# Optimization experiments

Hardware: AMD Instinct MI355X
Metric: run time of the kernel (lower is better)

## Reference

```python
import jax, jax.numpy as jnp
import numpy as np
from jax import lax

DIM = 384
NH = 8
HD = DIM // NH
M = 16          # num_anchors
B = 16
HH = 64
WW = 64
N = HH * WW
STD = 0.02


def setup_inputs() -> dict:
    key = jax.random.key(0)
    ks = jax.random.split(key, 12)
    rn = lambda k, shape: (jax.random.normal(k, shape, jnp.float32) * STD)
    return {
        "x": jax.random.normal(ks[0], (B, N, DIM), jnp.float32),
        "H": HH,
        "W": WW,
        "saliency_w": rn(ks[1], (DIM, 1)),
        "saliency_b": jnp.zeros((1,), jnp.float32),
        "anchor_seeds": rn(ks[2], (1, M, DIM)),
        "w_q_agg": rn(ks[3], (DIM, DIM)),
        "w_kv_agg": rn(ks[4], (DIM, 2 * DIM)),
        "w_q_self": rn(ks[5], (DIM, DIM)),
        "w_kv_self": rn(ks[6], (DIM, 2 * DIM)),
        "w_q_bcast": rn(ks[7], (DIM, DIM)),
        "w_kv_bcast": rn(ks[8], (DIM, 2 * DIM)),
        "dw_kernel": rn(ks[9], (DIM, 1, 3, 3)),  # depthwise conv, OIHW with I=1
        "w_proj": rn(ks[10], (DIM, DIM)),
    }


def _mhsa(q_in, kv_in, wq, wkv):
    """Multi-head cross attention. q_in: [B,Lq,C], kv_in: [B,Lk,C]."""
    b, lq, c = q_in.shape
    lk = kv_in.shape[1]
    scale = HD ** -0.5
    q = (q_in @ wq).reshape(b, lq, NH, HD)
    kv = (kv_in @ wkv).reshape(b, lk, 2, NH, HD)
    k, v = kv[:, :, 0], kv[:, :, 1]
    attn = jnp.einsum("bqhd,bkhd->bhqk", q, k) * scale
    attn = jax.nn.softmax(attn, axis=-1)
    out = jnp.einsum("bhqk,bkhd->bqhd", attn, v).reshape(b, lq, c)
    return out


def reference(x, H, W, saliency_w, saliency_b, anchor_seeds,
              w_q_agg, w_kv_agg, w_q_self, w_kv_self,
              w_q_bcast, w_kv_bcast, dw_kernel, w_proj):
    b, n, c = x.shape
    # saliency gating
    sal = jax.nn.sigmoid(x @ saliency_w + saliency_b)  # [B,N,1]
    x_sal = x * sal
    # stage 1: anchors aggregate from saliency-gated tokens
    anchors = jnp.broadcast_to(anchor_seeds, (b, M, c))
    anchors = anchors + _mhsa(anchors, x_sal, w_q_agg, w_kv_agg)
    # stage 2: anchor self-attention
    anchors = anchors + _mhsa(anchors, anchors, w_q_self, w_kv_self)
    # stage 3: broadcast anchors back to all tokens
    global_out = _mhsa(x, anchors, w_q_bcast, w_kv_bcast)
    # depthwise 3x3 conv on the 2D token map
    x2d = x.reshape(b, H, W, c).transpose(0, 3, 1, 2)  # NCHW
    local = lax.conv_general_dilated(
        x2d, dw_kernel, window_strides=(1, 1), padding="SAME",
        feature_group_count=c,
        dimension_numbers=("NCHW", "OIHW", "NCHW"))
    local = local.transpose(0, 2, 3, 1).reshape(b, n, c)
    return (global_out + local) @ w_proj
```

## Files before the change

kernel.cpp:

```cpp
#include <hip/hip_runtime.h>
#include <hip/hip_bf16.h>

#define SCALE 0.14433756729740643f

typedef __attribute__((ext_vector_type(8))) short bf16x8;
typedef __attribute__((ext_vector_type(4))) float f32x4;

template <typename T> __device__ inline T cvt_from_f(float v);
template <> __device__ inline float cvt_from_f<float>(float v) { return v; }
template <> __device__ inline __hip_bfloat16 cvt_from_f<__hip_bfloat16>(float v) { return __float2bfloat16(v); }

__device__ inline void gload16(const void* g, void* l) {
  __builtin_amdgcn_global_load_lds((const __attribute__((address_space(1))) void*)g,
                                   (__attribute__((address_space(3))) void*)l, 16, 0, 0);
}

__device__ inline int xcd_flat(int nwg) {
  int flat = (blockIdx.z * gridDim.y + blockIdx.y) * gridDim.x + blockIdx.x;
  int per = nwg >> 3;
  return (flat & 7) * per + (flat >> 3);
}

__global__ __launch_bounds__(256) void prep(const float* __restrict__ x,
                                            const float* __restrict__ wsal,
                                            const float* __restrict__ bsal,
                                            __hip_bfloat16* __restrict__ xb,
                                            float* __restrict__ sal) {
  int wave = threadIdx.x >> 6, lane = threadIdx.x & 63;
  size_t row = (size_t)blockIdx.x * 4 + wave;
  const float* xr = x + row * 384;
  float xs[6];
  float part = 0.f;
#pragma unroll
  for (int j = 0; j < 6; j++) {
    int c = lane + 64 * j;
    xs[j] = xr[c];
    part += xs[j] * wsal[c];
  }
#pragma unroll
  for (int off = 32; off >= 1; off >>= 1) part += __shfl_xor(part, off);
  float s = 1.f / (1.f + __expf(-(part + bsal[0])));
#pragma unroll
  for (int j = 0; j < 6; j++) {
    int c = lane + 64 * j;
    xb[row * 384 + c] = __float2bfloat16(xs[j]);
  }
  if (lane == 0) sal[row] = s;
}

__global__ void wcast_tv(const float* __restrict__ w, __hip_bfloat16* __restrict__ wt) {
  int idx = blockIdx.x * 256 + threadIdx.x;
  if (idx >= 384 * 384) return;
  int n = idx / 384, k = idx % 384;
  wt[idx] = __float2bfloat16(w[(size_t)k * 768 + 384 + n]);
}

template <int K, typename OT, int BSHIFT>
__global__ __launch_bounds__(256) void gemm_mfma(const __hip_bfloat16* __restrict__ A,
                                                 const __hip_bfloat16* __restrict__ BT,
                                                 OT* __restrict__ out, int Ncols,
                                                 size_t btBatchStride) {
  __shared__ __align__(16) __hip_bfloat16 Asl[128][32];
  __shared__ __align__(16) __hip_bfloat16 Bsl[128][32];
  int nf = xcd_flat(gridDim.x * gridDim.y);
  int bX = nf % gridDim.x, bY = nf / gridDim.x;
  int tid = threadIdx.x;
  int lane = tid & 63;
  int w = tid >> 6;
  int wr = w >> 1, wc = w & 1;
  int fr = lane & 15, fq = lane >> 4;
  int rowBase = bY * 128, colBase = bX * 128;
  const __hip_bfloat16* BTb = BT + (size_t)(rowBase >> BSHIFT) * btBatchStride;

  int r1 = tid >> 2, kc1 = tid & 3;
  int r2 = (tid + 256) >> 2;

  char* aB1 = (char*)Asl + (size_t)(w * 64) * 16;
  char* aB2 = (char*)Asl + (size_t)(256 + w * 64) * 16;
  char* bB1 = (char*)Bsl + (size_t)(w * 64) * 16;
  char* bB2 = (char*)Bsl + (size_t)(256 + w * 64) * 16;

  const __hip_bfloat16* a1 = A + (size_t)(rowBase + r1) * K + kc1 * 8;
  const __hip_bfloat16* a2 = A + (size_t)(rowBase + r2) * K + kc1 * 8;
  const __hip_bfloat16* b1 = BTb + (size_t)(colBase + r1) * K + kc1 * 8;
  const __hip_bfloat16* b2 = BTb + (size_t)(colBase + r2) * K + kc1 * 8;

  f32x4 acc[4][4] = {};

  for (int kk = 0; kk < K; kk += 32) {
    gload16(a1 + kk, aB1);
    gload16(a2 + kk, aB2);
    gload16(b1 + kk, bB1);
    gload16(b2 + kk, bB2);
    __syncthreads();
    bf16x8 af[4], bfv[4];
#pragma unroll
    for (int m = 0; m < 4; m++) af[m] = *(const bf16x8*)&Asl[wr * 64 + m * 16 + fr][fq * 8];
#pragma unroll
    for (int n = 0; n < 4; n++) bfv[n] = *(const bf16x8*)&Bsl[wc * 64 + n * 16 + fr][fq * 8];
#pragma unroll
    for (int m = 0; m < 4; m++)
#pragma unroll
      for (int n = 0; n < 4; n++)
        acc[m][n] = __builtin_amdgcn_mfma_f32_16x16x32_bf16(af[m], bfv[n], acc[m][n], 0, 0, 0);
    __syncthreads();
  }

#pragma unroll
  for (int m = 0; m < 4; m++) {
    int row0 = rowBase + wr * 64 + m * 16 + fq * 4;
#pragma unroll
    for (int n = 0; n < 4; n++) {
      int col = colBase + wc * 64 + n * 16 + fr;
      f32x4 v = acc[m][n];
#pragma unroll
      for (int r = 0; r < 4; r++) out[(size_t)(row0 + r) * Ncols + col] = cvt_from_f<OT>(v[r]);
    }
  }
}

__global__ __launch_bounds__(256) void gemm_logits(const __hip_bfloat16* __restrict__ A,
                                                   const __hip_bfloat16* __restrict__ BT,
                                                   __hip_bfloat16* __restrict__ lgT,
                                                   const float* __restrict__ rowScale) {
  constexpr int K = 384;
  __shared__ __align__(16) __hip_bfloat16 Asl[128][32];
  __shared__ __align__(16) __hip_bfloat16 Bsl[128][32];
  int tid = threadIdx.x;
  int lane = tid & 63;
  int w = tid >> 6;
  int wr = w >> 1, wc = w & 1;
  int fr = lane & 15, fq = lane >> 4;
  int rowBase = blockIdx.x * 128;

  int r1 = tid >> 2, kc1 = tid & 3;
  int r2 = (tid + 256) >> 2;

  char* aB1 = (char*)Asl + (size_t)(w * 64) * 16;
  char* aB2 = (char*)Asl + (size_t)(256 + w * 64) * 16;
  char* bB1 = (char*)Bsl + (size_t)(w * 64) * 16;
  char* bB2 = (char*)Bsl + (size_t)(256 + w * 64) * 16;

  const __hip_bfloat16* a1 = A + (size_t)(rowBase + r1) * K + kc1 * 8;
  const __hip_bfloat16* a2 = A + (size_t)(rowBase + r2) * K + kc1 * 8;
  const __hip_bfloat16* b1 = BT + (size_t)r1 * K + kc1 * 8;
  const __hip_bfloat16* b2 = BT + (size_t)r2 * K + kc1 * 8;

  f32x4 acc[4][4] = {};

  for (int kk = 0; kk < K; kk += 32) {
    gload16(a1 + kk, aB1);
    gload16(a2 + kk, aB2);
    gload16(b1 + kk, bB1);
    gload16(b2 + kk, bB2);
    __syncthreads();
    bf16x8 af[4], bfv[4];
#pragma unroll
    for (int m = 0; m < 4; m++) af[m] = *(const bf16x8*)&Asl[wr * 64 + m * 16 + fr][fq * 8];
#pragma unroll
    for (int n = 0; n < 4; n++) bfv[n] = *(const bf16x8*)&Bsl[wc * 64 + n * 16 + fr][fq * 8];
#pragma unroll
    for (int m = 0; m < 4; m++)
#pragma unroll
      for (int n = 0; n < 4; n++)
        acc[m][n] = __builtin_amdgcn_mfma_f32_16x16x32_bf16(af[m], bfv[n], acc[m][n], 0, 0, 0);
    __syncthreads();
  }

  float sv[4][4];
#pragma unroll
  for (int m = 0; m < 4; m++)
#pragma unroll
    for (int r = 0; r < 4; r++)
      sv[m][r] = rowScale[rowBase + wr * 64 + m * 16 + fq * 4 + r];

#pragma unroll
  for (int m = 0; m < 4; m++) {
    int row0 = rowBase + wr * 64 + m * 16 + fq * 4;
    int bb = row0 >> 12;
    int n0 = row0 & 4095;
#pragma unroll
    for (int n = 0; n < 4; n++) {
      int col = wc * 64 + n * 16 + fr;
      __hip_bfloat16 tb[4];
#pragma unroll
      for (int r = 0; r < 4; r++) tb[r] = __float2bfloat16(acc[m][n][r] * sv[m][r]);
      *(unsigned long long*)(lgT + ((size_t)bb * 128 + col) * 4096 + n0) = *(unsigned long long*)tb;
    }
  }
}

__global__ __launch_bounds__(256) void softmax_rows(const __hip_bfloat16* __restrict__ lgT,
                                                    const float* __restrict__ sal,
                                                    __hip_bfloat16* __restrict__ PT) {
  int g = blockIdx.x;
  const __hip_bfloat16* row = lgT + (size_t)g * 4096;
  int tid = threadIdx.x, wv = tid >> 6, lane = tid & 63;
  __shared__ float redm[4], reds[4];
  float v[16];
  union { ulonglong2 u; __hip_bfloat16 h[8]; } L0, L1;
  L0.u = *(const ulonglong2*)(row + tid * 16);
  L1.u = *(const ulonglong2*)(row + tid * 16 + 8);
#pragma unroll
  for (int i = 0; i < 8; i++) {
    v[i] = __bfloat162float(L0.h[i]);
    v[8 + i] = __bfloat162float(L1.h[i]);
  }
  float mx = v[0];
#pragma unroll
  for (int i = 1; i < 16; i++) mx = fmaxf(mx, v[i]);
#pragma unroll
  for (int off = 1; off < 64; off <<= 1) mx = fmaxf(mx, __shfl_xor(mx, off));
  if (lane == 0) redm[wv] = mx;
  __syncthreads();
  mx = fmaxf(fmaxf(redm[0], redm[1]), fmaxf(redm[2], redm[3]));
  float s = 0.f;
#pragma unroll
  for (int i = 0; i < 16; i++) {
    v[i] = __expf(v[i] - mx);
    s += v[i];
  }
#pragma unroll
  for (int off = 1; off < 64; off <<= 1) s += __shfl_xor(s, off);
  if (lane == 0) reds[wv] = s;
  __syncthreads();
  s = (reds[0] + reds[1]) + (reds[2] + reds[3]);
  float inv = 1.f / s;
  const float* sp = sal + (size_t)(g >> 7) * 4096 + tid * 16;
  float salv[16];
#pragma unroll
  for (int i = 0; i < 4; i++) {
    float4 q = *(const float4*)(sp + i * 4);
    salv[i * 4] = q.x; salv[i * 4 + 1] = q.y; salv[i * 4 + 2] = q.z; salv[i * 4 + 3] = q.w;
  }
  __hip_bfloat16 tb[16];
#pragma unroll
  for (int i = 0; i < 16; i++) tb[i] = __float2bfloat16(v[i] * inv * salv[i]);
  __hip_bfloat16* op = PT + (size_t)g * 4096 + tid * 16;
  *(ulonglong2*)op = *(ulonglong2*)tb;
  *(ulonglong2*)(op + 8) = *(ulonglong2*)(tb + 8);
}

__global__ __launch_bounds__(256) void gemm_pvx(const __hip_bfloat16* __restrict__ PT,
                                                const __hip_bfloat16* __restrict__ xb,
                                                float* __restrict__ pbuf) {
  __shared__ __align__(16) __hip_bfloat16 Asl[128][32];
  __shared__ __align__(16) short Bsl[128][40];
  int nf = xcd_flat(384);
  int bX = nf % 3, bY = (nf / 3) & 15, kz = nf / 48;
  int tid = threadIdx.x;
  int lane = tid & 63;
  int w = tid >> 6;
  int wr = w >> 1, wc = w & 1;
  int fr = lane & 15, fq = lane >> 4;
  int rowBase = bY * 128, colBase = bX * 128;

  int r1 = tid >> 2, kc1 = tid & 3;
  int r2 = (tid + 256) >> 2;
  char* aB1 = (char*)Asl + (size_t)(w * 64) * 16;
  char* aB2 = (char*)Asl + (size_t)(256 + w * 64) * 16;
  const __hip_bfloat16* a1 = PT + (size_t)(rowBase + r1) * 4096 + kz * 512 + kc1 * 8;
  const __hip_bfloat16* a2 = PT + (size_t)(rowBase + r2) * 4096 + kz * 512 + kc1 * 8;

  int nl1 = tid >> 4;
  int cc = tid & 15;
  const __hip_bfloat16* Bg0 = xb + ((size_t)bY * 4096 + kz * 512) * 384 + colBase + cc * 8;

  f32x4 acc[4][4] = {};

  for (int kk = 0; kk < 512; kk += 32) {
    gload16(a1 + kk, aB1);
    gload16(a2 + kk, aB2);
    const __hip_bfloat16* Bg = Bg0 + (size_t)kk * 384;
    bf16x8 rb1 = *(const bf16x8*)(Bg + (size_t)nl1 * 384);
    bf16x8 rb2 = *(const bf16x8*)(Bg + (size_t)(nl1 + 16) * 384);
#pragma unroll
    for (int j = 0; j < 8; j++) {
      Bsl[cc * 8 + j][nl1] = rb1[j];
      Bsl[cc * 8 + j][nl1 + 16] = rb2[j];
    }
    __syncthreads();
    bf16x8 af[4], bfv[4];
#pragma unroll
    for (int m = 0; m < 4; m++) af[m] = *(const bf16x8*)&Asl[wr * 64 + m * 16 + fr][fq * 8];
#pragma unroll
    for (int n = 0; n < 4; n++) bfv[n] = *(const bf16x8*)&Bsl[wc * 64 + n * 16 + fr][fq * 8];
#pragma unroll
    for (int m = 0; m < 4; m++)
#pragma unroll
      for (int n = 0; n < 4; n++)
        acc[m][n] = __builtin_amdgcn_mfma_f32_16x16x32_bf16(af[m], bfv[n], acc[m][n], 0, 0, 0);
    __syncthreads();
  }

  float* outz = pbuf + (size_t)kz * 786432;
#pragma unroll
  for (int m = 0; m < 4; m++) {
    int row0 = rowBase + wr * 64 + m * 16 + fq * 4;
#pragma unroll
    for (int n = 0; n < 4; n++) {
      int col = colBase + wc * 64 + n * 16 + fr;
      f32x4 v = acc[m][n];
#pragma unroll
      for (int r = 0; r < 4; r++) outz[(size_t)(row0 + r) * 384 + col] = v[r];
    }
  }
}

__global__ __launch_bounds__(256) void reduce_z(const float* __restrict__ pbuf,
                                                __hip_bfloat16* __restrict__ pvx) {
  int i4 = (blockIdx.x * 256 + threadIdx.x) * 4;
  float4 s = *(const float4*)(pbuf + i4);
#pragma unroll
  for (int z = 1; z < 8; z++) {
    float4 t = *(const float4*)(pbuf + (size_t)z * 786432 + i4);
    s.x += t.x; s.y += t.y; s.z += t.z; s.w += t.w;
  }
  __hip_bfloat16 tb[4] = {__float2bfloat16(s.x), __float2bfloat16(s.y),
                          __float2bfloat16(s.z), __float2bfloat16(s.w)};
  *(unsigned long long*)(pvx + i4) = *(unsigned long long*)tb;
}

__global__ void anch_fix(const float* __restrict__ outF, const float* __restrict__ seeds,
                         float* __restrict__ anch1) {
  int idx = blockIdx.x * 256 + threadIdx.x;
  int b = idx / 6144;
  int rem = idx - b * 6144;
  int m = rem / 384, c = rem - m * 384;
  int h = c / 48;
  anch1[idx] = seeds[rem] + outF[((size_t)b * 128 + h * 16 + m) * 384 + c];
}

__global__ void fill_wl(const float* __restrict__ wkv, const float* __restrict__ qseed,
                        __hip_bfloat16* __restrict__ wvlT) {
  int idx = blockIdx.x * 256 + threadIdx.x;
  int hm = idx / 384, ci = idx - hm * 384;
  int h = hm >> 4, m = hm & 15;
  const float* wp = wkv + (size_t)ci * 768 + h * 48;
  const float* qp = qseed + m * 384 + h * 48;
  float acc = 0.f;
#pragma unroll
  for (int d = 0; d < 48; d++) acc += wp[d] * qp[d];
  wvlT[384 * 384 + idx] = __float2bfloat16(acc);
}

__global__ __launch_bounds__(256) void wtrans(const float* __restrict__ wproj,
                                              __hip_bfloat16* __restrict__ bt2) {
  __shared__ float t[64][65];
  int kt = blockIdx.x * 64, ct = blockIdx.y * 64;
  int tid = threadIdx.x;
  int c = tid & 63, r4 = tid >> 6;
#pragma unroll
  for (int i = 0; i < 16; i++) {
    int r = i * 4 + r4;
    t[r][c] = wproj[(size_t)(kt + r) * 384 + ct + c];
  }
  __syncthreads();
  __hip_bfloat16 vals[16];
#pragma unroll
  for (int i = 0; i < 16; i++) vals[i] = __float2bfloat16(t[c][i * 4 + r4]);
  for (int b = blockIdx.z * 4; b < blockIdx.z * 4 + 4; b++) {
    __hip_bfloat16* dst = bt2 + (size_t)b * 196608;
#pragma unroll
    for (int i = 0; i < 16; i++) {
      int rr = i * 4 + r4;
      dst[(size_t)(ct + rr) * 512 + kt + c] = vals[i];
    }
  }
}

__global__ __launch_bounds__(256) void fill_fold(const float* __restrict__ wq,
                                                 const float* __restrict__ wproj,
                                                 const float* __restrict__ kvb,
                                                 __hip_bfloat16* __restrict__ wpbT,
                                                 __hip_bfloat16* __restrict__ bt2) {
  int b = blockIdx.y;
  int tid = threadIdx.x;
  __shared__ float stage[16][48];
  __shared__ __hip_bfloat16 obuf[16][264];
  if (blockIdx.x < 8) {
    int h = blockIdx.x;
    for (int idx = tid; idx < 768; idx += 256) {
      int m = idx / 48, d = idx % 48;
      stage[m][d] = kvb[(size_t)(b * 16 + m) * 768 + h * 48 + d];
    }
    __syncthreads();
    for (int kbase = 0; kbase < 384; kbase += 256) {
      int chunk = (kbase == 0) ? 256 : 128;
      if (tid < chunk) {
        int k = kbase + tid;
        const float4* wp = (const float4*)(wq + (size_t)k * 384 + h * 48);
        float acc[16] = {};
#pragma unroll
        for (int dq = 0; dq < 12; dq++) {
          float4 wv = wp[dq];
#pragma unroll
          for (int m = 0; m < 16; m++)
            acc[m] += stage[m][dq * 4] * wv.x + stage[m][dq * 4 + 1] * wv.y +
                      stage[m][dq * 4 + 2] * wv.z + stage[m][dq * 4 + 3] * wv.w;
        }
#pragma unroll
        for (int m = 0; m < 16; m++) obuf[m][tid] = __float2bfloat16(acc[m]);
      }
      __syncthreads();
      for (int widx = tid; widx < 16 * chunk; widx += 256) {
        int m = widx / chunk, kk = widx - m * chunk;
        wpbT[(size_t)b * 49152 + (size_t)(h * 16 + m) * 384 + kbase + kk] = obuf[m][kk];
      }
      __syncthreads();
    }
  } else {
    int h = blockIdx.x - 8;
    for (int idx = tid; idx < 768; idx += 256) {
      int m = idx / 48, d = idx % 48;
      stage[m][d] = kvb[(size_t)(b * 16 + m) * 768 + 384 + h * 48 + d];
    }
    __syncthreads();
    for (int cp = tid; cp < 384; cp += 256) {
      float acc[16] = {};
      for (int d = 0; d < 48; d++) {
        float wv = wproj[(size_t)(h * 48 + d) * 384 + cp];
#pragma unroll
        for (int m = 0; m < 16; m++) acc[m] += stage[m][d] * wv;
      }
      __hip_bfloat16 tb[16];
#pragma unroll
      for (int m = 0; m < 16; m++) tb[m] = __float2bfloat16(acc[m]);
      __hip_bfloat16* dst = bt2 + (size_t)b * 196608 + (size_t)cp * 512 + 384 + h * 16;
      *(ulonglong2*)dst = *(ulonglong2*)tb;
      *(ulonglong2*)(dst + 8) = *(ulonglong2*)(tb + 8);
    }
  }
}

__global__ __launch_bounds__(256) void pgemm(const __hip_bfloat16* __restrict__ A,
                                             const __hip_bfloat16* __restrict__ wpbT,
                                             __hip_bfloat16* __restrict__ A2) {
  constexpr int K = 384;
  __shared__ __align__(16) __hip_bfloat16 Asl[128][32];
  __shared__ __align__(16) __hip_bfloat16 Bsl[128][32];
  int tid = threadIdx.x;
  int lane = tid & 63;
  int w = tid >> 6;
  int wr = w >> 1, wc = w & 1;
  int fr = lane & 15, fq = lane >> 4;
  int rowBase = blockIdx.y * 128;
  const __hip_bfloat16* BTb = wpbT + (size_t)(rowBase >> 12) * (128 * 384);

  int r1 = tid >> 2, kc1 = tid & 3;
  int r2 = (tid + 256) >> 2;

  char* aB1 = (char*)Asl + (size_t)(w * 64) * 16;
  char* aB2 = (char*)Asl + (size_t)(256 + w * 64) * 16;
  char* bB1 = (char*)Bsl + (size_t)(w * 64) * 16;
  char* bB2 = (char*)Bsl + (size_t)(256 + w * 64) * 16;

  const __hip_bfloat16* a1 = A + (size_t)(rowBase + r1) * K + kc1 * 8;
  const __hip_bfloat16* a2 = A + (size_t)(rowBase + r2) * K + kc1 * 8;
  const __hip_bfloat16* b1 = BTb + (size_t)r1 * K + kc1 * 8;
  const __hip_bfloat16* b2 = BTb + (size_t)r2 * K + kc1 * 8;

  f32x4 acc[4][4] = {};

  for (int kk = 0; kk < K; kk += 32) {
    gload16(a1 + kk, aB1);
    gload16(a2 + kk, aB2);
    gload16(b1 + kk, bB1);
    gload16(b2 + kk, bB2);
    __syncthreads();
    bf16x8 af[4], bfv[4];
#pragma unroll
    for (int m = 0; m < 4; m++) af[m] = *(const bf16x8*)&Asl[wr * 64 + m * 16 + fr][fq * 8];
#pragma unroll
    for (int n = 0; n < 4; n++) bfv[n] = *(const bf16x8*)&Bsl[wc * 64 + n * 16 + fr][fq * 8];
#pragma unroll
    for (int m = 0; m < 4; m++)
#pragma unroll
      for (int n = 0; n < 4; n++)
        acc[m][n] = __builtin_amdgcn_mfma_f32_16x16x32_bf16(af[m], bfv[n], acc[m][n], 0, 0, 0);
    __syncthreads();
  }

#pragma unroll
  for (int m = 0; m < 4; m++) {
    int row0 = rowBase + wr * 64 + m * 16 + fq * 4;
#pragma unroll
    for (int n = 0; n < 4; n++) {
      int col = wc * 64 + n * 16 + fr;
      f32x4 v = acc[m][n];
      f32x4 mx = v;
#pragma unroll
      for (int off = 1; off < 16; off <<= 1)
#pragma unroll
        for (int r = 0; r < 4; r++) mx[r] = fmaxf(mx[r], __shfl_xor(mx[r], off));
      f32x4 e;
#pragma unroll
      for (int r = 0; r < 4; r++) e[r] = __expf(v[r] - mx[r]);
      f32x4 s = e;
#pragma unroll
      for (int off = 1; off < 16; off <<= 1)
#pragma unroll
        for (int r = 0; r < 4; r++) s[r] += __shfl_xor(s[r], off);
#pragma unroll
      for (int r = 0; r < 4; r++)
        A2[(size_t)(row0 + r) * 512 + 384 + col] = __float2bfloat16(e[r] / s[r]);
    }
  }
}

__global__ __launch_bounds__(256) void dwconv3(const __hip_bfloat16* __restrict__ xb,
                                               const float* __restrict__ dwk,
                                               __hip_bfloat16* __restrict__ A2) {
  int b = blockIdx.y;
  int y = blockIdx.x;
  int w = threadIdx.x >> 6, lane = threadIdx.x & 63;
  int c0 = lane * 6;
  int x0 = w * 16;
  float kw[9][6];
#pragma unroll
  for (int ki = 0; ki < 9; ki++)
#pragma unroll
    for (int i = 0; i < 6; i++) kw[ki][i] = dwk[(c0 + i) * 9 + ki];

  const __hip_bfloat16* base = xb + ((size_t)(b * 4096 + y * 64)) * 384 + c0;
  bool yv[3];
#pragma unroll
  for (int t = 0; t < 3; t++) {
    int yy = y + t - 1;
    yv[t] = (yy >= 0 && yy < 64);
  }

  float colL[3][6], colC[3][6], colR[3][6];
  auto loadcol = [&](float (&dst)[3][6], int x) {
#pragma unroll
    for (int t = 0; t < 3; t++) {
      if (yv[t]) {
        const __hip_bfloat16* p = base + ((size_t)(t - 1) * 64 + x) * 384;
#pragma unroll
        for (int i = 0; i < 6; i++) dst[t][i] = __bfloat162float(p[i]);
      } else {
#pragma unroll
        for (int i = 0; i < 6; i++) dst[t][i] = 0.f;
      }
    }
  };

  if (x0 == 0) {
#pragma unroll
    for (int t = 0; t < 3; t++)
#pragma unroll
      for (int i = 0; i < 6; i++) colL[t][i] = 0.f;
  } else {
    loadcol(colL, x0 - 1);
  }
  loadcol(colC, x0);

  for (int step = 0; step < 16; step++) {
    int x = x0 + step;
    if (x + 1 < 64) {
      loadcol(colR, x + 1);
    } else {
#pragma unroll
      for (int t = 0; t < 3; t++)
#pragma unroll
        for (int i = 0; i < 6; i++) colR[t][i] = 0.f;
    }
    float acc[6];
#pragma unroll
    for (int i = 0; i < 6; i++) {
      float a = 0.f;
#pragma unroll
      for (int t = 0; t < 3; t++)
        a += colL[t][i] * kw[t * 3 + 0][i] + colC[t][i] * kw[t * 3 + 1][i] +
             colR[t][i] * kw[t * 3 + 2][i];
      acc[i] = a;
    }
    __hip_bfloat16 tb[6];
#pragma unroll
    for (int i = 0; i < 6; i++) tb[i] = __float2bfloat16(acc[i]);
    __hip_bfloat16* gp = A2 + ((size_t)(b * 4096 + y * 64 + x)) * 512 + c0;
    *(unsigned int*)(gp) = *(unsigned int*)(tb);
    *(unsigned int*)(gp + 2) = *(unsigned int*)(tb + 2);
    *(unsigned int*)(gp + 4) = *(unsigned int*)(tb + 4);
#pragma unroll
    for (int t = 0; t < 3; t++)
#pragma unroll
      for (int i = 0; i < 6; i++) {
        colL[t][i] = colC[t][i];
        colC[t][i] = colR[t][i];
      }
  }
}

__global__ __launch_bounds__(256) void anchor_proj2(const float* __restrict__ A,
                                                    const float* __restrict__ W,
                                                    float* __restrict__ out, int wstride,
                                                    int scaleCols) {
  int cs = blockIdx.x * 16;
  int b = blockIdx.y;
  __shared__ float a1[16][385];
  int tid = threadIdx.x;
  for (int idx = tid; idx < 6144; idx += 256) a1[idx / 384][idx % 384] = A[b * 6144 + idx];
  __syncthreads();
  int m = tid >> 4, cc = tid & 15;
  int col = cs + cc;
  const float* wp = W + col;
  float acc0 = 0.f, acc1 = 0.f, acc2 = 0.f, acc3 = 0.f;
#pragma unroll 4
  for (int k = 0; k < 384; k += 4) {
    acc0 += a1[m][k] * wp[(size_t)k * wstride];
    acc1 += a1[m][k + 1] * wp[(size_t)(k + 1) * wstride];
    acc2 += a1[m][k + 2] * wp[(size_t)(k + 2) * wstride];
    acc3 += a1[m][k + 3] * wp[(size_t)(k + 3) * wstride];
  }
  float acc = (acc0 + acc1) + (acc2 + acc3);
  if (col < scaleCols) acc *= SCALE;
  out[((size_t)b * 16 + m) * wstride + col] = acc;
}

__global__ __launch_bounds__(256) void anchor_proj_qkv(const float* __restrict__ A,
                                                       const float* __restrict__ Wq,
                                                       const float* __restrict__ Wkv,
                                                       float* __restrict__ q_out,
                                                       float* __restrict__ kv_out) {
  bool isQ = blockIdx.x < 24;
  int bx = isQ ? blockIdx.x : blockIdx.x - 24;
  const float* W = isQ ? Wq : Wkv;
  float* outp = isQ ? q_out : kv_out;
  int wstride = isQ ? 384 : 768;
  float scale = isQ ? SCALE : 1.f;
  int cs = bx * 16;
  int b = blockIdx.y;
  __shared__ float a1[16][385];
  int tid = threadIdx.x;
  for (int idx = tid; idx < 6144; idx += 256) a1[idx / 384][idx % 384] = A[b * 6144 + idx];
  __syncthreads();
  int m = tid >> 4, cc = tid & 15;
  int col = cs + cc;
  const float* wp = W + col;
  float acc0 = 0.f, acc1 = 0.f, acc2 = 0.f, acc3 = 0.f;
#pragma unroll 4
  for (int k = 0; k < 384; k += 4) {
    acc0 += a1[m][k] * wp[(size_t)k * wstride];
    acc1 += a1[m][k + 1] * wp[(size_t)(k + 1) * wstride];
    acc2 += a1[m][k + 2] * wp[(size_t)(k + 2) * wstride];
    acc3 += a1[m][k + 3] * wp[(size_t)(k + 3) * wstride];
  }
  float acc = ((acc0 + acc1) + (acc2 + acc3)) * scale;
  outp[((size_t)b * 16 + m) * wstride + col] = acc;
}

__global__ void self_attn(const float* __restrict__ qsf, const float* __restrict__ kvs,
                          const float* __restrict__ anch1, float* __restrict__ anch2) {
  int h = blockIdx.x & 7, b = blockIdx.x >> 3;
  __shared__ float qs[16][48], ks[16][48], vs[16][48], p[16][17];
  int tid = threadIdx.x;
  for (int idx = tid; idx < 768; idx += 256) {
    int m = idx / 48, d = idx % 48;
    qs[m][d] = qsf[(b * 16 + m) * 384 + h * 48 + d];
    ks[m][d] = kvs[(b * 16 + m) * 768 + h * 48 + d];
    vs[m][d] = kvs[(b * 16 + m) * 768 + 384 + h * 48 + d];
  }
  __syncthreads();
  {
    int mq = tid >> 4, mk = tid & 15;
    float acc = 0.f;
    for (int d = 0; d < 48; d++) acc += qs[mq][d] * ks[mk][d];
    p[mq][mk] = acc;
  }
  __syncthreads();
  if (tid < 16) {
    float mx = -1e30f;
    for (int mk = 0; mk < 16; mk++) mx = fmaxf(mx, p[tid][mk]);
    float sum = 0.f;
    for (int mk = 0; mk < 16; mk++) {
      float e = __expf(p[tid][mk] - mx);
      p[tid][mk] = e;
      sum += e;
    }
    float inv = 1.f / sum;
    for (int mk = 0; mk < 16; mk++) p[tid][mk] *= inv;
  }
  __syncthreads();
  for (int idx = tid; idx < 768; idx += 256) {
    int m = idx / 48, d = idx % 48;
    float acc = 0.f;
    for (int mk = 0; mk < 16; mk++) acc += p[m][mk] * vs[mk][d];
    int c = h * 48 + d;
    anch2[(b * 16 + m) * 384 + c] = anch1[(b * 16 + m) * 384 + c] + acc;
  }
}

extern "C" void kernel_launch(void* const* d_in, const int* in_sizes, int n_in,
                              void* d_out, int out_size, void* d_ws, size_t ws_size,
                              hipStream_t stream) {
  (void)in_sizes; (void)n_in; (void)out_size; (void)ws_size;
  const float* x = (const float*)d_in[0];
  const float* wsal = (const float*)d_in[3];
  const float* bsal = (const float*)d_in[4];
  const float* seeds = (const float*)d_in[5];
  const float* w_q_agg = (const float*)d_in[6];
  const float* w_kv_agg = (const float*)d_in[7];
  const float* w_q_self = (const float*)d_in[8];
  const float* w_kv_self = (const float*)d_in[9];
  const float* w_q_bcast = (const float*)d_in[10];
  const float* w_kv_bcast = (const float*)d_in[11];
  const float* dwk = (const float*)d_in[12];
  const float* w_proj = (const float*)d_in[13];
  float* out = (float*)d_out;

  char* ws = (char*)d_ws;
  size_t off = 0;
  auto take = [&](size_t bytes) -> void* {
    void* p = ws + off;
    off += (bytes + 255) & ~(size_t)255;
    return p;
  };
  __hip_bfloat16* xb = (__hip_bfloat16*)take(50331648);
  char* R = (char*)take(67108864);
  __hip_bfloat16* PT = (__hip_bfloat16*)take(16777216);
  __hip_bfloat16* pvx = (__hip_bfloat16*)take(1572864);
  float* outF = (float*)take(3145728);
  float* qseed = (float*)take(24576);
  float* sal = (float*)take(262144);
  float* anch1 = (float*)take(393216);
  float* anch2 = (float*)take(393216);
  float* q_self = (float*)take(393216);
  float* kv_self = (float*)take(786432);
  float* kv_b = (float*)take(786432);
  __hip_bfloat16* wvlT = (__hip_bfloat16*)take(393216);
  __hip_bfloat16* wpbT = (__hip_bfloat16*)take(1572864);
  __hip_bfloat16* bt2 = (__hip_bfloat16*)take(6291456);
  __hip_bfloat16* logitsT = (__hip_bfloat16*)R;
  float* pbuf = (float*)R;
  __hip_bfloat16* A2 = (__hip_bfloat16*)R;

  prep<<<16384, 256, 0, stream>>>(x, wsal, bsal, xb, sal);
  anchor_proj2<<<dim3(24, 1), 256, 0, stream>>>(seeds, w_q_agg, qseed, 384, 384);
  wcast_tv<<<576, 256, 0, stream>>>(w_kv_agg, wvlT);
  fill_wl<<<192, 256, 0, stream>>>(w_kv_agg, qseed, wvlT);
  wtrans<<<dim3(6, 6, 4), 256, 0, stream>>>(w_proj, bt2);
  gemm_logits<<<512, 256, 0, stream>>>(xb, wvlT + 384 * 384, logitsT, sal);
  softmax_rows<<<2048, 256, 0, stream>>>(logitsT, sal, PT);
  gemm_pvx<<<dim3(3, 16, 8), 256, 0, stream>>>(PT, xb, pbuf);
  reduce_z<<<768, 256, 0, stream>>>(pbuf, pvx);
  gemm_mfma<384, float, 12><<<dim3(3, 16), 256, 0, stream>>>(pvx, wvlT, outF, 384, 0);
  anch_fix<<<384, 256, 0, stream>>>(outF, seeds, anch1);
  anchor_proj_qkv<<<dim3(72, 16), 256, 0, stream>>>(anch1, w_q_self, w_kv_self, q_self, kv_self);
  self_attn<<<128, 256, 0, stream>>>(q_self, kv_self, anch1, anch2);
  anchor_proj2<<<dim3(48, 16), 256, 0, stream>>>(anch2, w_kv_bcast, kv_b, 768, 384);
  fill_fold<<<dim3(16, 16), 256, 0, stream>>>(w_q_bcast, w_proj, kv_b, wpbT, bt2);
  pgemm<<<dim3(1, 512), 256, 0, stream>>>(xb, wpbT, A2);
  dwconv3<<<dim3(64, 16), 256, 0, stream>>>(xb, dwk, A2);
  gemm_mfma<512, float, 12><<<dim3(3, 512), 256, 0, stream>>>(A2, bt2, out, 384, (size_t)384 * 512);
}
```

Baseline: 350.6 us.

## Pre-transpose x to channel-major so PV GEMM loads B via direct-to-LDS

Adds an xtrans kernel that writes a channel-major bf16 copy of x, so gemm_pvx can fetch its B operand with global_load_lds like A instead of register loads and a scalar transpose scatter into LDS. The split-K factor is halved from 8 to 4 (K chunk 1024), which cuts partial-sum traffic and the reduce work. The cost is an extra full pass over x (read and write of about 50MB) plus a second 50MB workspace buffer, and fewer workgroups in the PV GEMM.

```diff
diff --git a/kernel.cpp b/kernel.cpp
--- a/kernel.cpp
+++ b/kernel.cpp
@@ -46,6 +46,36 @@
     xb[row * 384 + c] = __float2bfloat16(xs[j]);
   }
   if (lane == 0) sal[row] = s;
+}
+
+__global__ __launch_bounds__(256) void xtrans(const __hip_bfloat16* __restrict__ xb,
+                                              __hip_bfloat16* __restrict__ xbT) {
+  __shared__ short t[64][66];
+  int n0 = blockIdx.x * 64, c0 = blockIdx.y * 64, b = blockIdx.z;
+  int tid = threadIdx.x;
+  int r = tid >> 3, c8 = tid & 7;
+#pragma unroll
+  for (int i = 0; i < 2; i++) {
+    int row = r + i * 32;
+    bf16x8 v = *(const bf16x8*)(xb + ((size_t)(b * 4096 + n0 + row)) * 384 + c0 + c8 * 8);
+    unsigned int* trow = (unsigned int*)&t[row][c8 * 8];
+#pragma unroll
+    for (int j = 0; j < 4; j++) {
+      union { unsigned int u; short s[2]; } p;
+      p.s[0] = v[j * 2];
+      p.s[1] = v[j * 2 + 1];
+      trow[j] = p.u;
+    }
+  }
+  __syncthreads();
+#pragma unroll
+  for (int i = 0; i < 2; i++) {
+    int crow = r + i * 32;
+    short tb[8];
+#pragma unroll
+    for (int j = 0; j < 8; j++) tb[j] = t[c8 * 8 + j][crow];
+    *(ulonglong2*)(xbT + ((size_t)b * 384 + c0 + crow) * 4096 + n0 + c8 * 8) = *(ulonglong2*)tb;
+  }
 }
 
 __global__ void wcast_tv(const float* __restrict__ w, __hip_bfloat16* __restrict__ wt) {
@@ -242,11 +272,11 @@
 }
 
 __global__ __launch_bounds__(256) void gemm_pvx(const __hip_bfloat16* __restrict__ PT,
-                                                const __hip_bfloat16* __restrict__ xb,
+                                                const __hip_bfloat16* __restrict__ xbT,
                                                 float* __restrict__ pbuf) {
   __shared__ __align__(16) __hip_bfloat16 Asl[128][32];
-  __shared__ __align__(16) short Bsl[128][40];
-  int nf = xcd_flat(384);
+  __shared__ __align__(16) __hip_bfloat16 Bsl[128][32];
+  int nf = xcd_flat(192);
   int bX = nf % 3, bY = (nf / 3) & 15, kz = nf / 48;
   int tid = threadIdx.x;
   int lane = tid & 63;
@@ -254,31 +284,28 @@
   int wr = w >> 1, wc = w & 1;
   int fr = lane & 15, fq = lane >> 4;
   int rowBase = bY * 128, colBase = bX * 128;
+  const __hip_bfloat16* BTb = xbT + (size_t)bY * 384 * 4096;
 
   int r1 = tid >> 2, kc1 = tid & 3;
   int r2 = (tid + 256) >> 2;
+
   char* aB1 = (char*)Asl + (size_t)(w * 64) * 16;
   char* aB2 = (char*)Asl + (size_t)(256 + w * 64) * 16;
-  const __hip_bfloat16* a1 = PT + (size_t)(rowBase + r1) * 4096 + kz * 512 + kc1 * 8;
-  const __hip_bfloat16* a2 = PT + (size_t)(rowBase + r2) * 4096 + kz * 512 + kc1 * 8;
-
-  int nl1 = tid >> 4;
-  int cc = tid & 15;
-  const __hip_bfloat16* Bg0 = xb + ((size_t)bY * 4096 + kz * 512) * 384 + colBase + cc * 8;
+  char* bB1 = (char*)Bsl + (size_t)(w * 64) * 16;
+  char* bB2 = (char*)Bsl + (size_t)(256 + w * 64) * 16;
+
+  const __hip_bfloat16* a1 = PT + (size_t)(rowBase + r1) * 4096 + kz * 1024 + kc1 * 8;
+  const __hip_bfloat16* a2 = PT + (size_t)(rowBase + r2) * 4096 + kz * 1024 + kc1 * 8;
+  const __hip_bfloat16* b1 = BTb + (size_t)(colBase + r1) * 4096 + kz * 1024 + kc1 * 8;
+  const __hip_bfloat16* b2 = BTb + (size_t)(colBase + r2) * 4096 + kz * 1024 + kc1 * 8;
 
   f32x4 acc[4][4] = {};
 
-  for (int kk = 0; kk < 512; kk += 32) {
+  for (int kk = 0; kk < 1024; kk += 32) {
     gload16(a1 + kk, aB1);
     gload16(a2 + kk, aB2);
-    const __hip_bfloat16* Bg = Bg0 + (size_t)kk * 384;
-    bf16x8 rb1 = *(const bf16x8*)(Bg + (size_t)nl1 * 384);
-    bf16x8 rb2 = *(const bf16x8*)(Bg + (size_t)(nl1 + 16) * 384);
-#pragma unroll
-    for (int j = 0; j < 8; j++) {
-      Bsl[cc * 8 + j][nl1] = rb1[j];
-      Bsl[cc * 8 + j][nl1 + 16] = rb2[j];
-    }
+    gload16(b1 + kk, bB1);
+    gload16(b2 + kk, bB2);
     __syncthreads();
     bf16x8 af[4], bfv[4];
 #pragma unroll
@@ -312,7 +339,7 @@
   int i4 = (blockIdx.x * 256 + threadIdx.x) * 4;
   float4 s = *(const float4*)(pbuf + i4);
 #pragma unroll
-  for (int z = 1; z < 8; z++) {
+  for (int z = 1; z < 4; z++) {
     float4 t = *(const float4*)(pbuf + (size_t)z * 786432 + i4);
     s.x += t.x; s.y += t.y; s.z += t.z; s.w += t.w;
   }
@@ -717,6 +744,7 @@
     return p;
   };
   __hip_bfloat16* xb = (__hip_bfloat16*)take(50331648);
+  __hip_bfloat16* xbT = (__hip_bfloat16*)take(50331648);
   char* R = (char*)take(67108864);
   __hip_bfloat16* PT = (__hip_bfloat16*)take(16777216);
   __hip_bfloat16* pvx = (__hip_bfloat16*)take(1572864);
@@ -736,13 +764,14 @@
   __hip_bfloat16* A2 = (__hip_bfloat16*)R;
 
   prep<<<16384, 256, 0, stream>>>(x, wsal, bsal, xb, sal);
+  xtrans<<<dim3(64, 6, 16), 256, 0, stream>>>(xb, xbT);
   anchor_proj2<<<dim3(24, 1), 256, 0, stream>>>(seeds, w_q_agg, qseed, 384, 384);
   wcast_tv<<<576, 256, 0, stream>>>(w_kv_agg, wvlT);
   fill_wl<<<192, 256, 0, stream>>>(w_kv_agg, qseed, wvlT);
   wtrans<<<dim3(6, 6, 4), 256, 0, stream>>>(w_proj, bt2);
   gemm_logits<<<512, 256, 0, stream>>>(xb, wvlT + 384 * 384, logitsT, sal);
   softmax_rows<<<2048, 256, 0, stream>>>(logitsT, sal, PT);
-  gemm_pvx<<<dim3(3, 16, 8), 256, 0, stream>>>(PT, xb, pbuf);
+  gemm_pvx<<<dim3(3, 16, 4), 256, 0, stream>>>(PT, xbT, pbuf);
   reduce_z<<<768, 256, 0, stream>>>(pbuf, pvx);
   gemm_mfma<384, float, 12><<<dim3(3, 16), 256, 0, stream>>>(pvx, wvlT, outF, 384, 0);
   anch_fix<<<384, 256, 0, stream>>>(outF, seeds, anch1);
```

New measurement: 352.7 us. Within noise of the previous version (+0.6%).
